# Kernel tuning notes

Measured on AMD Instinct MI355X. Metric: run time of the kernel, lower is better.

The kernel has to match this reference:

```python
import jax, jax.numpy as jnp
import numpy as np

D_MODEL = 512
EPS = 1e-5  # torch LayerNorm default


def _layernorm(x, g, b):
    mu = jnp.mean(x, axis=-1, keepdims=True)
    var = jnp.mean(jnp.square(x - mu), axis=-1, keepdims=True)
    return (x - mu) * jax.lax.rsqrt(var + EPS) * g + b


def setup_inputs() -> dict:
    key = jax.random.key(0)
    ks = jax.random.split(key, 12)
    d = D_MODEL
    s = 1.0 / np.sqrt(d)
    s4 = 1.0 / np.sqrt(4 * d)
    return {
        "x": jax.random.normal(ks[0], (4, 4096, d), dtype=jnp.float32),
        "Wq": jax.random.uniform(ks[1], (d, d), jnp.float32, -s, s),
        "bq": jax.random.uniform(ks[2], (d,), jnp.float32, -s, s),
        "Wk": jax.random.uniform(ks[3], (d, d), jnp.float32, -s, s),
        "bk": jax.random.uniform(ks[4], (d,), jnp.float32, -s, s),
        "Wv": jax.random.uniform(ks[5], (d, d), jnp.float32, -s, s),
        "bv": jax.random.uniform(ks[6], (d,), jnp.float32, -s, s),
        "g1": jnp.ones((d,), jnp.float32),
        "b1": jnp.zeros((d,), jnp.float32),
        "g2": jnp.ones((d,), jnp.float32),
        "b2": jnp.zeros((d,), jnp.float32),
        "W1": jax.random.uniform(ks[7], (d, 4 * d), jnp.float32, -s, s),
        "bf1": jax.random.uniform(ks[8], (4 * d,), jnp.float32, -s, s),
        "W2": jax.random.uniform(ks[9], (4 * d, d), jnp.float32, -s4, s4),
        "bf2": jax.random.uniform(ks[10], (d,), jnp.float32, -s4, s4),
    }


def reference(x, Wq, bq, Wk, bk, Wv, bv, g1, b1, g2, b2, W1, bf1, W2, bf2):
    # QKV projections: [b, s, d]
    Q = jnp.einsum("bsd,de->bse", x, Wq) + bq
    K = jnp.einsum("bsd,de->bse", x, Wk) + bk
    V = jnp.einsum("bsd,de->bse", x, Wv) + bv
    scale = 1.0 / jnp.sqrt(jnp.float32(K.shape[-1]))
    scores = jnp.einsum("bqd,bkd->bqk", Q, K) * scale  # [b, s, s]
    attn = jax.nn.softmax(scores, axis=-1)
    att = jnp.einsum("bqk,bkd->bqd", attn, V)
    x = _layernorm(x + att, g1, b1)
    h = jax.nn.relu(jnp.einsum("bsd,df->bsf", x, W1) + bf1)
    ffn = jnp.einsum("bsf,fd->bsd", h, W2) + bf2
    return _layernorm(x + ffn, g2, b2)
```

## Files before the change

### kernel.cpp

```cpp
#include <hip/hip_runtime.h>
#include <hip/hip_bf16.h>

typedef unsigned short u16;
typedef short bf16x8 __attribute__((ext_vector_type(8)));
typedef float f32x4 __attribute__((ext_vector_type(4)));

__device__ __forceinline__ float b2f(u16 u) {
  union { float f; unsigned int i; } v; v.i = ((unsigned int)u) << 16; return v.f;
}
__device__ __forceinline__ u16 f2b(float f) {
  union { float f; unsigned int i; } v; v.f = f;
  unsigned int r = v.i + 0x7fffu + ((v.i >> 16) & 1u);
  return (u16)(r >> 16);
}
__device__ __forceinline__ u16 to_b(float v) { return f2b(v); }
__device__ __forceinline__ u16 to_b(u16 v) { return v; }
__device__ __forceinline__ float to_f(float v) { return v; }
__device__ __forceinline__ float to_f(u16 v) { return b2f(v); }

__device__ __forceinline__ void gl_lds16(const u16* g, u16* l) {
  __builtin_amdgcn_global_load_lds(
      (const __attribute__((address_space(1))) unsigned int*)g,
      (__attribute__((address_space(3))) unsigned int*)l, 16, 0, 0);
}

template <bool RELU, bool ATOMIC>
__global__ __launch_bounds__(256)
void gemm_nt(const u16* __restrict__ A, const u16* __restrict__ Bt,
             const float* __restrict__ bias, void* __restrict__ Cv,
             int N, int K, int nsplit, int lda, int ldb, int ldc,
             long sA, long sB, long sC, float scale) {
  __shared__ __align__(16) u16 As[128 * 64];
  __shared__ __align__(16) u16 Bs[128 * 64];
  const int z = blockIdx.z;
  const int batch = z / nsplit, split = z - batch * nsplit;
  const int Ks = K / nsplit;
  const u16* Ab = A + (long)batch * sA + (long)split * Ks;
  const u16* Bb = Bt + (long)batch * sB + (long)split * Ks;
  const int m0 = blockIdx.y * 128, n0 = blockIdx.x * 128;
  const int t = threadIdx.x, w = t >> 6, lane = t & 63;
  const int wm = (w >> 1) * 64, wn = (w & 1) * 64;
  const int lr = lane & 15, q = lane >> 4;

  int srow[4], scol[4];
#pragma unroll
  for (int i = 0; i < 4; i++) {
    int n = w * 256 + i * 64 + lane;
    srow[i] = n >> 3;
    scol[i] = (((n & 7) ^ ((n >> 3) & 7)) * 8);
  }

  f32x4 acc[4][4];
#pragma unroll
  for (int i = 0; i < 4; i++)
#pragma unroll
    for (int j = 0; j < 4; j++) acc[i][j] = (f32x4){0.f, 0.f, 0.f, 0.f};

  for (int k0 = 0; k0 < Ks; k0 += 64) {
#pragma unroll
    for (int i = 0; i < 4; i++) {
      u16* ldst = &As[(w * 256 + i * 64) * 8];
      gl_lds16(Ab + (long)(m0 + srow[i]) * lda + k0 + scol[i], ldst);
    }
#pragma unroll
    for (int i = 0; i < 4; i++) {
      u16* ldst = &Bs[(w * 256 + i * 64) * 8];
      gl_lds16(Bb + (long)(n0 + srow[i]) * ldb + k0 + scol[i], ldst);
    }
    __syncthreads();
#pragma unroll
    for (int kk = 0; kk < 2; kk++) {
      bf16x8 af[4], bfr[4];
#pragma unroll
      for (int i = 0; i < 4; i++) {
        int row = wm + i * 16 + lr;
        int phys = (kk * 4 + q) ^ (row & 7);
        af[i] = *(const bf16x8*)&As[row * 64 + phys * 8];
      }
#pragma unroll
      for (int j = 0; j < 4; j++) {
        int row = wn + j * 16 + lr;
        int phys = (kk * 4 + q) ^ (row & 7);
        bfr[j] = *(const bf16x8*)&Bs[row * 64 + phys * 8];
      }
#pragma unroll
      for (int i = 0; i < 4; i++)
#pragma unroll
        for (int j = 0; j < 4; j++)
          acc[i][j] = __builtin_amdgcn_mfma_f32_16x16x32_bf16(af[i], bfr[j], acc[i][j], 0, 0, 0);
    }
    __syncthreads();
  }

#pragma unroll
  for (int j = 0; j < 4; j++) {
    int cg = n0 + wn + j * 16 + lr;
    float bb = (!ATOMIC && bias) ? bias[cg] : 0.0f;
#pragma unroll
    for (int i = 0; i < 4; i++) {
      int rbase = m0 + wm + i * 16 + q * 4;
#pragma unroll
      for (int r = 0; r < 4; r++) {
        float vv = acc[i][j][r] * scale;
        if (ATOMIC) {
          atomicAdd((float*)Cv + (long)batch * sC + (long)(rbase + r) * ldc + cg, vv);
        } else {
          vv += bb;
          if (RELU) vv = fmaxf(vv, 0.0f);
          ((u16*)Cv)[(long)batch * sC + (long)(rbase + r) * ldc + cg] = f2b(vv);
        }
      }
    }
  }
}

template <typename TS>
__global__ __launch_bounds__(1024)
void transpose_b(const TS* __restrict__ src, u16* __restrict__ dst,
                 int R, int Cc, int src_ld, long sbs, long dbs) {
  __shared__ u16 tile[32][33];
  int r = blockIdx.y * 32 + threadIdx.y;
  int c = blockIdx.x * 32 + threadIdx.x;
  tile[threadIdx.y][threadIdx.x] = to_b(src[(long)blockIdx.z * sbs + (long)r * src_ld + c]);
  __syncthreads();
  int rr = blockIdx.x * 32 + threadIdx.y;
  int cc = blockIdx.y * 32 + threadIdx.x;
  dst[(long)blockIdx.z * dbs + (long)rr * R + cc] = tile[threadIdx.x][threadIdx.y];
}

__global__ __launch_bounds__(256)
void f32_to_bf16(const float* __restrict__ s, u16* __restrict__ d) {
  long i = ((long)blockIdx.x * 256 + threadIdx.x) * 8;
  float4 a0 = *(const float4*)(s + i);
  float4 a1 = *(const float4*)(s + i + 4);
  u16 tmp[8] = {f2b(a0.x), f2b(a0.y), f2b(a0.z), f2b(a0.w),
                f2b(a1.x), f2b(a1.y), f2b(a1.z), f2b(a1.w)};
  *(uint4*)(d + i) = *(uint4*)tmp;
}

__global__ __launch_bounds__(256)
void softmax_inplace(u16* __restrict__ S) {
  const int row = blockIdx.x;
  u16* p = S + (size_t)row * 4096;
  const int t = threadIdx.x;
  float v[16];
  float mx = -1e30f;
#pragma unroll
  for (int i = 0; i < 16; i++) { v[i] = b2f(p[t + i * 256]); mx = fmaxf(mx, v[i]); }
#pragma unroll
  for (int o = 32; o > 0; o >>= 1) mx = fmaxf(mx, __shfl_xor(mx, o));
  __shared__ float red[4];
  int w = t >> 6;
  if ((t & 63) == 0) red[w] = mx;
  __syncthreads();
  mx = fmaxf(fmaxf(red[0], red[1]), fmaxf(red[2], red[3]));
  __syncthreads();
  float s = 0.f;
#pragma unroll
  for (int i = 0; i < 16; i++) { v[i] = __expf(v[i] - mx); s += v[i]; }
#pragma unroll
  for (int o = 32; o > 0; o >>= 1) s += __shfl_xor(s, o);
  if ((t & 63) == 0) red[w] = s;
  __syncthreads();
  s = red[0] + red[1] + red[2] + red[3];
  float inv = 1.0f / s;
#pragma unroll
  for (int i = 0; i < 16; i++) p[t + i * 256] = f2b(v[i] * inv);
}

template <typename TX, typename TR, bool EB, typename TO>
__global__ __launch_bounds__(256)
void add_ln(const TX* __restrict__ X, const TR* __restrict__ Rr,
            const float* __restrict__ eb,
            const float* __restrict__ g, const float* __restrict__ b,
            TO* __restrict__ O) {
  const int row = blockIdx.x * 4 + (threadIdx.x >> 6);
  const int lane = threadIdx.x & 63;
  const size_t base = (size_t)row * 512 + lane * 8;
  float z[8];
  float s1 = 0.f, s2 = 0.f;
#pragma unroll
  for (int i = 0; i < 8; i++) {
    int c = lane * 8 + i;
    z[i] = to_f(X[base + i]) + to_f(Rr[base + i]) + (EB ? eb[c] : 0.0f);
    s1 += z[i]; s2 += z[i] * z[i];
  }
#pragma unroll
  for (int o = 32; o > 0; o >>= 1) { s1 += __shfl_xor(s1, o); s2 += __shfl_xor(s2, o); }
  const float mu = s1 * (1.0f / 512.0f);
  const float var = s2 * (1.0f / 512.0f) - mu * mu;
  const float rstd = rsqrtf(var + 1e-5f);
#pragma unroll
  for (int i = 0; i < 8; i++) {
    int c = lane * 8 + i;
    float vv = (z[i] - mu) * rstd * g[c] + b[c];
    if (sizeof(TO) == 2) ((u16*)O)[base + i] = f2b(vv);
    else ((float*)O)[base + i] = vv;
  }
}

__global__ __launch_bounds__(256)
void concat3(const float* __restrict__ a, const float* __restrict__ b,
             const float* __restrict__ c, float* __restrict__ o) {
  int i = threadIdx.x + blockIdx.x * 256;
  if (i < 512) o[i] = a[i];
  else if (i < 1024) o[i] = b[i - 512];
  else if (i < 1536) o[i] = c[i - 1024];
}

extern "C" void kernel_launch(void* const* d_in, const int* in_sizes, int n_in,
                              void* d_out, int out_size, void* d_ws, size_t ws_size,
                              hipStream_t stream) {
  const float* x   = (const float*)d_in[0];
  const float* Wq  = (const float*)d_in[1];
  const float* bq  = (const float*)d_in[2];
  const float* Wk  = (const float*)d_in[3];
  const float* bk  = (const float*)d_in[4];
  const float* Wv  = (const float*)d_in[5];
  const float* bv  = (const float*)d_in[6];
  const float* g1  = (const float*)d_in[7];
  const float* b1  = (const float*)d_in[8];
  const float* g2  = (const float*)d_in[9];
  const float* b2  = (const float*)d_in[10];
  const float* W1  = (const float*)d_in[11];
  const float* bf1 = (const float*)d_in[12];
  const float* W2  = (const float*)d_in[13];
  const float* bf2 = (const float*)d_in[14];
  float* out = (float*)d_out;

  char* ws = (char*)d_ws;
  const size_t MB = 1048576;
  u16*   QKV   = (u16*)(ws + 0);
  u16*   Vt    = (u16*)(ws + 48 * MB);
  u16*   sc    = (u16*)(ws + 64 * MB);
  u16*   h     = sc;
  float* attf  = (float*)(ws + 128 * MB);
  float* ffnf  = attf;
  u16*   xb    = (u16*)(ws + 128 * MB);
  u16*   x1    = (u16*)(ws + 160 * MB);
  u16*   wqkvt = (u16*)(ws + 176 * MB);
  u16*   w1t   = wqkvt + 1536 * 512;
  u16*   w2t   = w1t + 2048 * 512;
  float* bqkv  = (float*)(w2t + 512 * 2048);

  dim3 tb(32, 32);
  f32_to_bf16<<<4096, 256, 0, stream>>>(x, xb);
  transpose_b<float><<<dim3(16, 16, 1), tb, 0, stream>>>(Wq, wqkvt,              512, 512, 512, 0, 0);
  transpose_b<float><<<dim3(16, 16, 1), tb, 0, stream>>>(Wk, wqkvt + 512 * 512,  512, 512, 512, 0, 0);
  transpose_b<float><<<dim3(16, 16, 1), tb, 0, stream>>>(Wv, wqkvt + 1024 * 512, 512, 512, 512, 0, 0);
  transpose_b<float><<<dim3(64, 16, 1), tb, 0, stream>>>(W1, w1t, 512, 2048, 2048, 0, 0);
  transpose_b<float><<<dim3(16, 64, 1), tb, 0, stream>>>(W2, w2t, 2048, 512, 512, 0, 0);
  concat3<<<6, 256, 0, stream>>>(bq, bk, bv, bqkv);

  gemm_nt<false, false><<<dim3(12, 128, 1), 256, 0, stream>>>(
      xb, wqkvt, bqkv, QKV, 1536, 512, 1, 512, 512, 1536, 0, 0, 0, 1.0f);

  transpose_b<u16><<<dim3(16, 128, 4), tb, 0, stream>>>(
      QKV + 1024, Vt, 4096, 512, 1536, 4096L * 1536, 512L * 4096);

  hipMemsetAsync(attf, 0, 32 * MB, stream);

  const float scl = 0.044194173824159216f;
  for (int b2i = 0; b2i < 4; b2i += 2) {
    const u16* Qp = QKV + (long)b2i * 4096 * 1536;
    const u16* Kp = Qp + 512;
    gemm_nt<false, false><<<dim3(32, 32, 2), 256, 0, stream>>>(
        Qp, Kp, nullptr, sc, 4096, 512, 1,
        1536, 1536, 4096, 4096L * 1536, 4096L * 1536, 4096L * 4096, scl);
    softmax_inplace<<<8192, 256, 0, stream>>>(sc);
    gemm_nt<false, true><<<dim3(4, 32, 4), 256, 0, stream>>>(
        sc, Vt + (long)b2i * 512 * 4096, nullptr, attf + (long)b2i * 4096 * 512,
        512, 4096, 2, 4096, 4096, 512, 4096L * 4096, 512L * 4096, 4096L * 512, 1.0f);
  }

  add_ln<float, float, false, u16><<<4096, 256, 0, stream>>>(x, attf, nullptr, g1, b1, x1);
  gemm_nt<true, false><<<dim3(16, 128, 1), 256, 0, stream>>>(
      x1, w1t, bf1, h, 2048, 512, 1, 512, 512, 2048, 0, 0, 0, 1.0f);
  hipMemsetAsync(ffnf, 0, 32 * MB, stream);
  gemm_nt<false, true><<<dim3(4, 128, 2), 256, 0, stream>>>(
      h, w2t, nullptr, ffnf, 512, 2048, 2, 2048, 2048, 512, 0, 0, 0, 1.0f);
  add_ln<u16, float, true, float><<<4096, 256, 0, stream>>>(x1, ffnf, bf2, g2, b2, out);
}
```

Baseline: 609.7 us.

## Fuse QK^T, softmax and PV into a single flash-attention kernel

Replaces the materialized 4096x4096 score GEMM, the in-place softmax kernel and the PV GEMM with one fused kernel. The fused kernel streams K and V tiles through LDS, computes exp scores in registers, feeds bf16 P through a per-wave LDS buffer into MFMA, and splits the KV range into two halves. The halves combine unnormalized outputs and row sums with atomics, and the division by the sum is folded into the first add+LayerNorm. This removes the large score-matrix round trips through HBM and several launches. It skips the running-max subtraction, so very large scores could overflow, and it adds atomic contention and unpipelined LDS loads with frequent barriers.

New measurement: 649.1 us. 1.06x slower.

```diff
diff --git a/kernel.cpp b/kernel.cpp
--- a/kernel.cpp
+++ b/kernel.cpp
@@ -58,15 +58,11 @@
 
   for (int k0 = 0; k0 < Ks; k0 += 64) {
 #pragma unroll
-    for (int i = 0; i < 4; i++) {
-      u16* ldst = &As[(w * 256 + i * 64) * 8];
-      gl_lds16(Ab + (long)(m0 + srow[i]) * lda + k0 + scol[i], ldst);
-    }
-#pragma unroll
-    for (int i = 0; i < 4; i++) {
-      u16* ldst = &Bs[(w * 256 + i * 64) * 8];
-      gl_lds16(Bb + (long)(n0 + srow[i]) * ldb + k0 + scol[i], ldst);
-    }
+    for (int i = 0; i < 4; i++)
+      gl_lds16(Ab + (long)(m0 + srow[i]) * lda + k0 + scol[i], &As[(w * 256 + i * 64) * 8]);
+#pragma unroll
+    for (int i = 0; i < 4; i++)
+      gl_lds16(Bb + (long)(n0 + srow[i]) * ldb + k0 + scol[i], &Bs[(w * 256 + i * 64) * 8]);
     __syncthreads();
 #pragma unroll
     for (int kk = 0; kk < 2; kk++) {
@@ -74,14 +70,12 @@
 #pragma unroll
       for (int i = 0; i < 4; i++) {
         int row = wm + i * 16 + lr;
-        int phys = (kk * 4 + q) ^ (row & 7);
-        af[i] = *(const bf16x8*)&As[row * 64 + phys * 8];
+        af[i] = *(const bf16x8*)&As[row * 64 + (((kk * 4 + q) ^ (row & 7)) * 8)];
       }
 #pragma unroll
       for (int j = 0; j < 4; j++) {
         int row = wn + j * 16 + lr;
-        int phys = (kk * 4 + q) ^ (row & 7);
-        bfr[j] = *(const bf16x8*)&Bs[row * 64 + phys * 8];
+        bfr[j] = *(const bf16x8*)&Bs[row * 64 + (((kk * 4 + q) ^ (row & 7)) * 8)];
       }
 #pragma unroll
       for (int i = 0; i < 4; i++)
@@ -112,6 +106,110 @@
       }
     }
   }
+}
+
+__global__ __launch_bounds__(256, 2)
+void flash_attn(const u16* __restrict__ QKV, const u16* __restrict__ Vt,
+                float* __restrict__ attf, float* __restrict__ lbuf, float scl) {
+  __shared__ __align__(16) u16 Ks[128 * 128];
+  __shared__ __align__(16) u16 Vs[64 * 128];
+  __shared__ __align__(16) u16 Ps[4 * 16 * 132];
+  const int qt = blockIdx.x;
+  const int half = blockIdx.y;
+  const int batch = blockIdx.z;
+  const int t = threadIdx.x, w = t >> 6, lane = t & 63;
+  const int lr = lane & 15, q = lane >> 4;
+  const long rowbase = (long)batch * 4096 + qt * 64;
+  const u16* Qrow  = QKV + (rowbase + w * 16 + lr) * 1536;
+  const u16* Kbase = QKV + ((long)batch * 4096 + half * 2048) * 1536 + 512;
+  const u16* Vtb   = Vt + (long)batch * 512 * 4096 + half * 2048;
+  u16* Pw = Ps + w * (16 * 132);
+
+  f32x4 O[32];
+#pragma unroll
+  for (int i = 0; i < 32; i++) O[i] = (f32x4){0.f, 0.f, 0.f, 0.f};
+  float lsum[4] = {0.f, 0.f, 0.f, 0.f};
+
+  for (int kv = 0; kv < 16; kv++) {
+    const int kv0 = kv * 128;
+    f32x4 S[8];
+#pragma unroll
+    for (int j = 0; j < 8; j++) S[j] = (f32x4){0.f, 0.f, 0.f, 0.f};
+
+    for (int kc = 0; kc < 4; kc++) {
+#pragma unroll
+      for (int rr = 0; rr < 8; rr++) {
+        int n = rr * 256 + t;
+        int row = n >> 4, c = (n & 15) ^ ((n >> 4) & 15);
+        gl_lds16(Kbase + (long)(kv0 + row) * 1536 + kc * 128 + c * 8,
+                 &Ks[(rr * 256 + w * 64) * 8]);
+      }
+      bf16x8 Qf[4];
+#pragma unroll
+      for (int ss = 0; ss < 4; ss++)
+        Qf[ss] = *(const bf16x8*)(Qrow + kc * 128 + ss * 32 + q * 8);
+      __syncthreads();
+#pragma unroll
+      for (int ss = 0; ss < 4; ss++)
+#pragma unroll
+        for (int j = 0; j < 8; j++) {
+          int row = j * 16 + lr;
+          bf16x8 Kf = *(const bf16x8*)&Ks[row * 128 + (((ss * 4 + q) ^ lr) * 8)];
+          S[j] = __builtin_amdgcn_mfma_f32_16x16x32_bf16(Qf[ss], Kf, S[j], 0, 0, 0);
+        }
+      __syncthreads();
+    }
+
+    float psum[4] = {0.f, 0.f, 0.f, 0.f};
+#pragma unroll
+    for (int j = 0; j < 8; j++)
+#pragma unroll
+      for (int r = 0; r < 4; r++) {
+        float e = __expf(S[j][r] * scl);
+        psum[r] += e;
+        Pw[(q * 4 + r) * 132 + j * 16 + lr] = f2b(e);
+      }
+#pragma unroll
+    for (int r = 0; r < 4; r++) {
+#pragma unroll
+      for (int o = 1; o < 16; o <<= 1) psum[r] += __shfl_xor(psum[r], o);
+      lsum[r] += psum[r];
+    }
+    bf16x8 Pf[4];
+#pragma unroll
+    for (int t4 = 0; t4 < 4; t4++)
+      Pf[t4] = *(const bf16x8*)&Pw[lr * 132 + t4 * 32 + q * 8];
+
+    for (int dc = 0; dc < 8; dc++) {
+#pragma unroll
+      for (int rr = 0; rr < 4; rr++) {
+        int n = rr * 256 + t;
+        int row = n >> 4, c = (n & 15) ^ ((n >> 4) & 15);
+        gl_lds16(Vtb + (long)(dc * 64 + row) * 4096 + kv0 + c * 8,
+                 &Vs[(rr * 256 + w * 64) * 8]);
+      }
+      __syncthreads();
+#pragma unroll
+      for (int t4 = 0; t4 < 4; t4++)
+#pragma unroll
+        for (int j = 0; j < 4; j++) {
+          int row = j * 16 + lr;
+          bf16x8 Vf = *(const bf16x8*)&Vs[row * 128 + (((t4 * 4 + q) ^ lr) * 8)];
+          O[dc * 4 + j] = __builtin_amdgcn_mfma_f32_16x16x32_bf16(Pf[t4], Vf, O[dc * 4 + j], 0, 0, 0);
+        }
+      __syncthreads();
+    }
+  }
+
+#pragma unroll
+  for (int i = 0; i < 32; i++)
+#pragma unroll
+    for (int r = 0; r < 4; r++)
+      atomicAdd(&attf[(rowbase + w * 16 + q * 4 + r) * 512 + i * 16 + lr], O[i][r]);
+  if (lr == 0)
+#pragma unroll
+    for (int r = 0; r < 4; r++)
+      atomicAdd(&lbuf[rowbase + w * 16 + q * 4 + r], lsum[r]);
 }
 
 template <typename TS>
@@ -138,51 +236,22 @@
   *(uint4*)(d + i) = *(uint4*)tmp;
 }
 
-__global__ __launch_bounds__(256)
-void softmax_inplace(u16* __restrict__ S) {
-  const int row = blockIdx.x;
-  u16* p = S + (size_t)row * 4096;
-  const int t = threadIdx.x;
-  float v[16];
-  float mx = -1e30f;
-#pragma unroll
-  for (int i = 0; i < 16; i++) { v[i] = b2f(p[t + i * 256]); mx = fmaxf(mx, v[i]); }
-#pragma unroll
-  for (int o = 32; o > 0; o >>= 1) mx = fmaxf(mx, __shfl_xor(mx, o));
-  __shared__ float red[4];
-  int w = t >> 6;
-  if ((t & 63) == 0) red[w] = mx;
-  __syncthreads();
-  mx = fmaxf(fmaxf(red[0], red[1]), fmaxf(red[2], red[3]));
-  __syncthreads();
-  float s = 0.f;
-#pragma unroll
-  for (int i = 0; i < 16; i++) { v[i] = __expf(v[i] - mx); s += v[i]; }
-#pragma unroll
-  for (int o = 32; o > 0; o >>= 1) s += __shfl_xor(s, o);
-  if ((t & 63) == 0) red[w] = s;
-  __syncthreads();
-  s = red[0] + red[1] + red[2] + red[3];
-  float inv = 1.0f / s;
-#pragma unroll
-  for (int i = 0; i < 16; i++) p[t + i * 256] = f2b(v[i] * inv);
-}
-
-template <typename TX, typename TR, bool EB, typename TO>
+template <typename TX, typename TR, bool EB, bool DIV, typename TO>
 __global__ __launch_bounds__(256)
 void add_ln(const TX* __restrict__ X, const TR* __restrict__ Rr,
-            const float* __restrict__ eb,
+            const float* __restrict__ lvec, const float* __restrict__ eb,
             const float* __restrict__ g, const float* __restrict__ b,
             TO* __restrict__ O) {
   const int row = blockIdx.x * 4 + (threadIdx.x >> 6);
   const int lane = threadIdx.x & 63;
   const size_t base = (size_t)row * 512 + lane * 8;
+  const float inv = DIV ? (1.0f / lvec[row]) : 1.0f;
   float z[8];
   float s1 = 0.f, s2 = 0.f;
 #pragma unroll
   for (int i = 0; i < 8; i++) {
     int c = lane * 8 + i;
-    z[i] = to_f(X[base + i]) + to_f(Rr[base + i]) + (EB ? eb[c] : 0.0f);
+    z[i] = to_f(X[base + i]) + to_f(Rr[base + i]) * inv + (EB ? eb[c] : 0.0f);
     s1 += z[i]; s2 += z[i] * z[i];
   }
 #pragma unroll
@@ -232,8 +301,8 @@
   const size_t MB = 1048576;
   u16*   QKV   = (u16*)(ws + 0);
   u16*   Vt    = (u16*)(ws + 48 * MB);
-  u16*   sc    = (u16*)(ws + 64 * MB);
-  u16*   h     = sc;
+  float* lbuf  = (float*)(ws + 64 * MB);
+  u16*   h     = (u16*)(ws + 64 * MB);
   float* attf  = (float*)(ws + 128 * MB);
   float* ffnf  = attf;
   u16*   xb    = (u16*)(ws + 128 * MB);
@@ -259,25 +328,18 @@
       QKV + 1024, Vt, 4096, 512, 1536, 4096L * 1536, 512L * 4096);
 
   hipMemsetAsync(attf, 0, 32 * MB, stream);
+  hipMemsetAsync(lbuf, 0, 16384 * sizeof(float), stream);
 
   const float scl = 0.044194173824159216f;
-  for (int b2i = 0; b2i < 4; b2i += 2) {
-    const u16* Qp = QKV + (long)b2i * 4096 * 1536;
-    const u16* Kp = Qp + 512;
-    gemm_nt<false, false><<<dim3(32, 32, 2), 256, 0, stream>>>(
-        Qp, Kp, nullptr, sc, 4096, 512, 1,
-        1536, 1536, 4096, 4096L * 1536, 4096L * 1536, 4096L * 4096, scl);
-    softmax_inplace<<<8192, 256, 0, stream>>>(sc);
-    gemm_nt<false, true><<<dim3(4, 32, 4), 256, 0, stream>>>(
-        sc, Vt + (long)b2i * 512 * 4096, nullptr, attf + (long)b2i * 4096 * 512,
-        512, 4096, 2, 4096, 4096, 512, 4096L * 4096, 512L * 4096, 4096L * 512, 1.0f);
-  }
-
-  add_ln<float, float, false, u16><<<4096, 256, 0, stream>>>(x, attf, nullptr, g1, b1, x1);
+  flash_attn<<<dim3(64, 2, 4), 256, 0, stream>>>(QKV, Vt, attf, lbuf, scl);
+
+  add_ln<float, float, false, true, u16><<<4096, 256, 0, stream>>>(
+      x, attf, lbuf, nullptr, g1, b1, x1);
   gemm_nt<true, false><<<dim3(16, 128, 1), 256, 0, stream>>>(
       x1, w1t, bf1, h, 2048, 512, 1, 512, 512, 2048, 0, 0, 0, 1.0f);
   hipMemsetAsync(ffnf, 0, 32 * MB, stream);
   gemm_nt<false, true><<<dim3(4, 128, 2), 256, 0, stream>>>(
       h, w2t, nullptr, ffnf, 512, 2048, 2, 2048, 2048, 512, 0, 0, 0, 1.0f);
-  add_ln<u16, float, true, float><<<4096, 256, 0, stream>>>(x1, ffnf, bf2, g2, b2, out);
-}
+  add_ln<u16, float, true, false, float><<<4096, 256, 0, stream>>>(
+      x1, ffnf, nullptr, bf2, g2, b2, out);
+}
```
